# Kernel tuning notes

Measured on AMD Instinct MI355X. Metric: run time of the kernel, lower is better.

The kernel has to match this reference:

```python
import jax, jax.numpy as jnp
import numpy as np

B, A, C, M = 8, 100000, 80, 32
ALPHA, GAMMA = 0.25, 2.0


def setup_inputs() -> dict:
    key = jax.random.key(0)
    k1, k2, k3, k4, k5, k6, k7 = jax.random.split(key, 7)
    cls = jax.random.uniform(k1, (B, A, C), jnp.float32, 1e-3, 1.0 - 1e-3)
    reg = jax.random.normal(k2, (B, A, 4), jnp.float32)
    # anchors: valid boxes with width/height in [16, 256]
    ctr = jax.random.uniform(k3, (A, 2), jnp.float32, 0.0, 800.0)
    wh = jax.random.uniform(k4, (A, 2), jnp.float32, 16.0, 256.0)
    anchors = jnp.concatenate([ctr - wh / 2, ctr + wh / 2], -1)[None]  # [1,A,4]
    # annotations: [B,M,5] = (x1,y1,x2,y2,class); class=-1 marks padding
    gctr = jax.random.uniform(k5, (B, M, 2), jnp.float32, 0.0, 800.0)
    gwh = jax.random.uniform(k6, (B, M, 2), jnp.float32, 32.0, 300.0)
    boxes = jnp.concatenate([gctr - gwh / 2, gctr + gwh / 2], -1)
    labels = jax.random.randint(k7, (B, M), 0, C).astype(jnp.float32)
    labels = labels.at[:, M - 8:].set(-1.0)  # padded GT rows
    annotations = jnp.concatenate([boxes, labels[..., None]], -1)
    return {"classifications": cls, "regressions": reg,
            "anchors": anchors, "annotations": annotations}


def _calc_iou(a, b):
    # a: [A,4] anchors, b: [M,4] gt boxes -> [A,M]
    area_a = (a[:, 2] - a[:, 0]) * (a[:, 3] - a[:, 1])
    area_b = (b[:, 2] - b[:, 0]) * (b[:, 3] - b[:, 1])
    iw = jnp.clip(jnp.minimum(a[:, 2, None], b[None, :, 2]) -
                  jnp.maximum(a[:, 0, None], b[None, :, 0]), 0.0)
    ih = jnp.clip(jnp.minimum(a[:, 3, None], b[None, :, 3]) -
                  jnp.maximum(a[:, 1, None], b[None, :, 1]), 0.0)
    inter = iw * ih
    ua = jnp.clip(area_a[:, None] + area_b[None, :] - inter, 1e-8)
    return inter / ua


def _per_image(cls, reg, anchor, ann):
    valid = ann[:, 4] >= 0.0                     # padded rows (class == -1)
    any_valid = valid.any()
    cls = jnp.clip(cls, 1e-4, 1.0 - 1e-4)
    iou = jnp.where(valid[None, :], _calc_iou(anchor, ann[:, :4]), -1.0)  # [A,M]
    iou_max = iou.max(1)
    iou_argmax = iou.argmax(1)
    pos = iou_max >= 0.5
    num_pos = pos.sum().astype(cls.dtype)
    assigned = ann[iou_argmax]                   # [A,5] gathered GT per anchor
    # build targets: -1 = ignore, 0 = negative, 1 = matched class
    targets = jnp.full(cls.shape, -1.0, cls.dtype)
    targets = jnp.where((iou_max < 0.4)[:, None], 0.0, targets)
    targets = jnp.where(pos[:, None], 0.0, targets)
    onehot = jax.nn.one_hot(assigned[:, 4].astype(jnp.int32), cls.shape[1], dtype=cls.dtype)
    targets = jnp.where(pos[:, None] & (onehot > 0), 1.0, targets)
    # focal loss
    alpha_factor = jnp.where(targets == 1.0, ALPHA, 1.0 - ALPHA)
    focal_w = alpha_factor * jnp.where(targets == 1.0, 1.0 - cls, cls) ** GAMMA
    bce = -(targets * jnp.log(cls) + (1.0 - targets) * jnp.log(1.0 - cls))
    cls_loss = jnp.where(targets != -1.0, focal_w * bce, 0.0).sum() / jnp.maximum(num_pos, 1.0)
    aw = anchor[:, 2] - anchor[:, 0]
    ah = anchor[:, 3] - anchor[:, 1]
    acx = anchor[:, 0] + 0.5 * aw
    acy = anchor[:, 1] + 0.5 * ah
    gw0 = assigned[:, 2] - assigned[:, 0]
    gh0 = assigned[:, 3] - assigned[:, 1]
    gcx = assigned[:, 0] + 0.5 * gw0
    gcy = assigned[:, 1] + 0.5 * gh0
    gw = jnp.clip(gw0, 1.0)
    gh = jnp.clip(gh0, 1.0)
    t = jnp.stack([(gcx - acx) / aw, (gcy - acy) / ah,
                   jnp.log(gw / aw), jnp.log(gh / ah)], axis=1)
    t = t / jnp.array([0.1, 0.1, 0.2, 0.2], cls.dtype)
    diff = jnp.abs(t - reg)
    sl1 = jnp.where(diff <= 1.0 / 9.0, 0.5 * 9.0 * diff ** 2, diff - 0.5 / 9.0)
    reg_loss = jnp.where(pos[:, None], sl1, 0.0).sum() / jnp.maximum(4.0 * num_pos, 1.0)
    reg_loss = jnp.where(num_pos > 0, reg_loss, 0.0)
    return (jnp.where(any_valid, cls_loss, 0.0),
            jnp.where(any_valid, reg_loss, 0.0))


def reference(classifications, regressions, anchors, annotations):
    anchor = anchors[0]
    cl, rl = jax.vmap(lambda c, r, a: _per_image(c, r, anchor, a))(
        classifications, regressions, annotations)
    return (jnp.mean(cl).reshape(1), jnp.mean(rl).reshape(1))
```

## Files before the change

### kernel.cpp

```cpp
#include <hip/hip_runtime.h>

#define A_N 100000
#define B_N 8
#define C_N 80
#define M_N 32
#define BLK 320
#define APB 320
#define NBLK 313

typedef float f32x4 __attribute__((ext_vector_type(4)));

#define NSLOT 64

__device__ __forceinline__ void elem4(f32x4 v, float wgt, float& acc) {
    float s4 = v.x*v.x*__logf(1.f - v.x) + v.y*v.y*__logf(1.f - v.y)
             + v.z*v.z*__logf(1.f - v.z) + v.w*v.w*__logf(1.f - v.w);
    acc = fmaf(-wgt, s4, acc);
}

__global__ __launch_bounds__(BLK) void focal_main(
    const float* __restrict__ cls,
    const float* __restrict__ regs,
    const float* __restrict__ anchors,
    const float* __restrict__ ann,
    float* __restrict__ ws)
{
    __shared__ float sAnn[M_N * 5];
    __shared__ float sW[APB];
    __shared__ float sRed[15];

    const int b          = blockIdx.y;
    const int blockStart = blockIdx.x * APB;
    const int tid        = threadIdx.x;
    const int a          = blockStart + tid;

    if (tid < M_N * 5) sAnn[tid] = ann[b * M_N * 5 + tid];
    __syncthreads();

    float clsPart = 0.f, regPart = 0.f, nposPart = 0.f;
    float pHit = 0.5f;
    int   meta = -2;

    if (a < A_N) {
        float4 an = reinterpret_cast<const float4*>(anchors)[a];
        float areaA = (an.z - an.x) * (an.w - an.y);
        float best = -1e30f;
        int bestIdx = 0;
        #pragma unroll
        for (int m = 0; m < M_N; ++m) {
            float gx1 = sAnn[m*5+0], gy1 = sAnn[m*5+1];
            float gx2 = sAnn[m*5+2], gy2 = sAnn[m*5+3];
            float gl  = sAnn[m*5+4];
            float iouv;
            if (gl >= 0.f) {
                float areaB = (gx2 - gx1) * (gy2 - gy1);
                float iw = fmaxf(fminf(an.z, gx2) - fmaxf(an.x, gx1), 0.f);
                float ih = fmaxf(fminf(an.w, gy2) - fmaxf(an.y, gy1), 0.f);
                float inter = iw * ih;
                float ua = fmaxf(areaA + areaB - inter, 1e-8f);
                iouv = inter / ua;
            } else {
                iouv = -1.f;
            }
            if (iouv > best) { best = iouv; bestIdx = m; }
        }
        bool pos = best >= 0.5f;
        bool neg = best <  0.4f;
        meta = pos ? (int)sAnn[bestIdx*5+4] : (neg ? -1 : -2);

        if (pos) {
            nposPart = 1.f;
            float ph = cls[((size_t)b * A_N + a) * C_N + meta];
            pHit = ph;

            float4 rg = reinterpret_cast<const float4*>(regs)[(size_t)b * A_N + a];
            float gx1 = sAnn[bestIdx*5+0], gy1 = sAnn[bestIdx*5+1];
            float gx2 = sAnn[bestIdx*5+2], gy2 = sAnn[bestIdx*5+3];
            float aw = an.z - an.x, ah = an.w - an.y;
            float acx = an.x + 0.5f * aw, acy = an.y + 0.5f * ah;
            float gw0 = gx2 - gx1, gh0 = gy2 - gy1;
            float gcx = gx1 + 0.5f * gw0, gcy = gy1 + 0.5f * gh0;
            float gw = fmaxf(gw0, 1.f), gh = fmaxf(gh0, 1.f);
            float t0 = ((gcx - acx) / aw) * 10.f;
            float t1 = ((gcy - acy) / ah) * 10.f;
            float t2 = __logf(gw / aw) * 5.f;
            float t3 = __logf(gh / ah) * 5.f;
            float d0 = fabsf(t0 - rg.x), d1 = fabsf(t1 - rg.y);
            float d2 = fabsf(t2 - rg.z), d3 = fabsf(t3 - rg.w);
            #define SL1(d) ((d) <= (1.f/9.f) ? 4.5f*(d)*(d) : (d) - (0.5f/9.f))
            regPart = SL1(d0) + SL1(d1) + SL1(d2) + SL1(d3);
            #undef SL1
        }
    }
    sW[tid] = (meta == -2) ? 0.f : 0.75f;
    __syncthreads();

    const int tD = tid / 20;
    const f32x4* cls4 = reinterpret_cast<const f32x4*>(
        cls + ((size_t)b * A_N + blockStart) * C_N);

    if (blockIdx.x != NBLK - 1) {
        #pragma unroll
        for (int k = 0; k < 20; k += 4) {
            f32x4 v0 = __builtin_nontemporal_load(&cls4[(k + 0) * BLK + tid]);
            f32x4 v1 = __builtin_nontemporal_load(&cls4[(k + 1) * BLK + tid]);
            f32x4 v2 = __builtin_nontemporal_load(&cls4[(k + 2) * BLK + tid]);
            f32x4 v3 = __builtin_nontemporal_load(&cls4[(k + 3) * BLK + tid]);
            float w0 = sW[tD + ((k + 0) << 4)];
            float w1 = sW[tD + ((k + 1) << 4)];
            float w2 = sW[tD + ((k + 2) << 4)];
            float w3 = sW[tD + ((k + 3) << 4)];
            elem4(v0, w0, clsPart);
            elem4(v1, w1, clsPart);
            elem4(v2, w2, clsPart);
            elem4(v3, w3, clsPart);
        }
    } else {
        #pragma unroll
        for (int k = 0; k < 20; ++k) {
            int al = tD + (k << 4);
            if (blockStart + al < A_N) {
                f32x4 v = __builtin_nontemporal_load(&cls4[k * BLK + tid]);
                elem4(v, sW[al], clsPart);
            }
        }
    }

    if (meta >= 0) {
        float om = 1.f - pHit;
        clsPart += -0.25f * om * om * __logf(pHit)
                   + 0.75f * pHit * pHit * __logf(om);
    }

    #pragma unroll
    for (int off = 32; off > 0; off >>= 1) {
        clsPart  += __shfl_down(clsPart,  off);
        regPart  += __shfl_down(regPart,  off);
        nposPart += __shfl_down(nposPart, off);
    }
    const int wid = tid >> 6;
    if ((tid & 63) == 0) {
        sRed[wid]      = clsPart;
        sRed[5 + wid]  = regPart;
        sRed[10 + wid] = nposPart;
    }
    __syncthreads();
    if (tid == 0) {
        const int slot = ((blockIdx.x & 7) << 3) | b;
        float c = sRed[0] + sRed[1] + sRed[2] + sRed[3] + sRed[4];
        float r = sRed[5] + sRed[6] + sRed[7] + sRed[8] + sRed[9];
        float n = sRed[10] + sRed[11] + sRed[12] + sRed[13] + sRed[14];
        atomicAdd(&ws[slot],             c);
        atomicAdd(&ws[NSLOT + slot],     r);
        atomicAdd(&ws[2 * NSLOT + slot], n);
    }
}

__global__ void focal_final(const float* __restrict__ ann,
                            const float* __restrict__ ws,
                            float* __restrict__ out)
{
    if (threadIdx.x == 0 && blockIdx.x == 0) {
        float cSum = 0.f, rSum = 0.f;
        for (int b = 0; b < B_N; ++b) {
            bool anyv = false;
            for (int m = 0; m < M_N; ++m)
                anyv = anyv || (ann[b * M_N * 5 + m * 5 + 4] >= 0.f);
            float cl = 0.f, rl = 0.f, np = 0.f;
            for (int k = 0; k < 8; ++k) {
                cl += ws[(k << 3) | b];
                rl += ws[NSLOT + ((k << 3) | b)];
                np += ws[2 * NSLOT + ((k << 3) | b)];
            }
            cl = cl / fmaxf(np, 1.f);
            rl = rl / fmaxf(4.f * np, 1.f);
            if (np <= 0.f) rl = 0.f;
            if (!anyv) { cl = 0.f; rl = 0.f; }
            cSum += cl;
            rSum += rl;
        }
        out[0] = cSum / (float)B_N;
        out[1] = rSum / (float)B_N;
    }
}

extern "C" void kernel_launch(void* const* d_in, const int* in_sizes, int n_in,
                              void* d_out, int out_size, void* d_ws, size_t ws_size,
                              hipStream_t stream) {
    const float* cls     = (const float*)d_in[0];
    const float* regs    = (const float*)d_in[1];
    const float* anchors = (const float*)d_in[2];
    const float* ann     = (const float*)d_in[3];
    float* out = (float*)d_out;
    float* ws  = (float*)d_ws;

    (void)hipMemsetAsync(ws, 0, 3 * NSLOT * sizeof(float), stream);

    dim3 grid(NBLK, B_N);
    focal_main<<<grid, BLK, 0, stream>>>(cls, regs, anchors, ann, ws);
    focal_final<<<1, 64, 0, stream>>>(ann, ws, out);
}
```

Measured before the change: 67.71 us.

## Prefetch first class tiles before IoU and drop atomics and memset

The first four nontemporal class-score vector loads are issued before the annotation barrier and the IoU matching loop, so their memory latency overlaps the matching compute. Per-block partial sums are now written to distinct workspace slots instead of being atomically added to 64 shared slots. This removes the hipMemsetAsync launch and the atomic contention. The final kernel becomes a 256-thread parallel reduction over all block slots, in exchange for holding more live registers through the IoU loop.

```diff
diff --git a/kernel.cpp b/kernel.cpp
--- a/kernel.cpp
+++ b/kernel.cpp
@@ -7,10 +7,9 @@
 #define BLK 320
 #define APB 320
 #define NBLK 313
+#define NSLOT (NBLK * B_N)
 
 typedef float f32x4 __attribute__((ext_vector_type(4)));
-
-#define NSLOT 64
 
 __device__ __forceinline__ void elem4(f32x4 v, float wgt, float& acc) {
     float s4 = v.x*v.x*__logf(1.f - v.x) + v.y*v.y*__logf(1.f - v.y)
@@ -33,8 +32,20 @@
     const int blockStart = blockIdx.x * APB;
     const int tid        = threadIdx.x;
     const int a          = blockStart + tid;
+    const bool full      = (blockIdx.x != NBLK - 1);
 
     if (tid < M_N * 5) sAnn[tid] = ann[b * M_N * 5 + tid];
+
+    const int tD = tid / 20;
+    const f32x4* cls4 = reinterpret_cast<const f32x4*>(
+        cls + ((size_t)b * A_N + blockStart) * C_N);
+    f32x4 v0, v1, v2, v3;
+    if (full) {
+        v0 = __builtin_nontemporal_load(&cls4[0 * BLK + tid]);
+        v1 = __builtin_nontemporal_load(&cls4[1 * BLK + tid]);
+        v2 = __builtin_nontemporal_load(&cls4[2 * BLK + tid]);
+        v3 = __builtin_nontemporal_load(&cls4[3 * BLK + tid]);
+    }
     __syncthreads();
 
     float clsPart = 0.f, regPart = 0.f, nposPart = 0.f;
@@ -70,8 +81,7 @@
 
         if (pos) {
             nposPart = 1.f;
-            float ph = cls[((size_t)b * A_N + a) * C_N + meta];
-            pHit = ph;
+            pHit = cls[((size_t)b * A_N + a) * C_N + meta];
 
             float4 rg = reinterpret_cast<const float4*>(regs)[(size_t)b * A_N + a];
             float gx1 = sAnn[bestIdx*5+0], gy1 = sAnn[bestIdx*5+1];
@@ -95,25 +105,25 @@
     sW[tid] = (meta == -2) ? 0.f : 0.75f;
     __syncthreads();
 
-    const int tD = tid / 20;
-    const f32x4* cls4 = reinterpret_cast<const f32x4*>(
-        cls + ((size_t)b * A_N + blockStart) * C_N);
-
-    if (blockIdx.x != NBLK - 1) {
-        #pragma unroll
-        for (int k = 0; k < 20; k += 4) {
-            f32x4 v0 = __builtin_nontemporal_load(&cls4[(k + 0) * BLK + tid]);
-            f32x4 v1 = __builtin_nontemporal_load(&cls4[(k + 1) * BLK + tid]);
-            f32x4 v2 = __builtin_nontemporal_load(&cls4[(k + 2) * BLK + tid]);
-            f32x4 v3 = __builtin_nontemporal_load(&cls4[(k + 3) * BLK + tid]);
+    if (full) {
+        elem4(v0, sW[tD + (0 << 4)], clsPart);
+        elem4(v1, sW[tD + (1 << 4)], clsPart);
+        elem4(v2, sW[tD + (2 << 4)], clsPart);
+        elem4(v3, sW[tD + (3 << 4)], clsPart);
+        #pragma unroll
+        for (int k = 4; k < 20; k += 4) {
+            f32x4 u0 = __builtin_nontemporal_load(&cls4[(k + 0) * BLK + tid]);
+            f32x4 u1 = __builtin_nontemporal_load(&cls4[(k + 1) * BLK + tid]);
+            f32x4 u2 = __builtin_nontemporal_load(&cls4[(k + 2) * BLK + tid]);
+            f32x4 u3 = __builtin_nontemporal_load(&cls4[(k + 3) * BLK + tid]);
             float w0 = sW[tD + ((k + 0) << 4)];
             float w1 = sW[tD + ((k + 1) << 4)];
             float w2 = sW[tD + ((k + 2) << 4)];
             float w3 = sW[tD + ((k + 3) << 4)];
-            elem4(v0, w0, clsPart);
-            elem4(v1, w1, clsPart);
-            elem4(v2, w2, clsPart);
-            elem4(v3, w3, clsPart);
+            elem4(u0, w0, clsPart);
+            elem4(u1, w1, clsPart);
+            elem4(u2, w2, clsPart);
+            elem4(u3, w3, clsPart);
         }
     } else {
         #pragma unroll
@@ -146,41 +156,54 @@
     }
     __syncthreads();
     if (tid == 0) {
-        const int slot = ((blockIdx.x & 7) << 3) | b;
-        float c = sRed[0] + sRed[1] + sRed[2] + sRed[3] + sRed[4];
-        float r = sRed[5] + sRed[6] + sRed[7] + sRed[8] + sRed[9];
-        float n = sRed[10] + sRed[11] + sRed[12] + sRed[13] + sRed[14];
-        atomicAdd(&ws[slot],             c);
-        atomicAdd(&ws[NSLOT + slot],     r);
-        atomicAdd(&ws[2 * NSLOT + slot], n);
-    }
-}
-
-__global__ void focal_final(const float* __restrict__ ann,
-                            const float* __restrict__ ws,
-                            float* __restrict__ out)
+        const int slot = blockIdx.x * B_N + b;
+        ws[slot]             = sRed[0] + sRed[1] + sRed[2] + sRed[3] + sRed[4];
+        ws[NSLOT + slot]     = sRed[5] + sRed[6] + sRed[7] + sRed[8] + sRed[9];
+        ws[2 * NSLOT + slot] = sRed[10] + sRed[11] + sRed[12] + sRed[13] + sRed[14];
+    }
+}
+
+__global__ __launch_bounds__(256) void focal_final(
+    const float* __restrict__ ann,
+    const float* __restrict__ ws,
+    float* __restrict__ out)
 {
-    if (threadIdx.x == 0 && blockIdx.x == 0) {
-        float cSum = 0.f, rSum = 0.f;
-        for (int b = 0; b < B_N; ++b) {
-            bool anyv = false;
-            for (int m = 0; m < M_N; ++m)
-                anyv = anyv || (ann[b * M_N * 5 + m * 5 + 4] >= 0.f);
-            float cl = 0.f, rl = 0.f, np = 0.f;
-            for (int k = 0; k < 8; ++k) {
-                cl += ws[(k << 3) | b];
-                rl += ws[NSLOT + ((k << 3) | b)];
-                np += ws[2 * NSLOT + ((k << 3) | b)];
-            }
-            cl = cl / fmaxf(np, 1.f);
-            rl = rl / fmaxf(4.f * np, 1.f);
-            if (np <= 0.f) rl = 0.f;
-            if (!anyv) { cl = 0.f; rl = 0.f; }
-            cSum += cl;
-            rSum += rl;
-        }
-        out[0] = cSum / (float)B_N;
-        out[1] = rSum / (float)B_N;
+    __shared__ float sC[8], sR[8];
+    const int tid = threadIdx.x;
+    const int g   = tid >> 5;
+    const int j   = tid & 31;
+
+    float c = 0.f, r = 0.f, n = 0.f;
+    for (int bx = j; bx < NBLK; bx += 32) {
+        int slot = bx * B_N + g;
+        c += ws[slot];
+        r += ws[NSLOT + slot];
+        n += ws[2 * NSLOT + slot];
+    }
+    #pragma unroll
+    for (int off = 16; off > 0; off >>= 1) {
+        c += __shfl_down(c, off, 32);
+        r += __shfl_down(r, off, 32);
+        n += __shfl_down(n, off, 32);
+    }
+    if (j == 0) {
+        bool anyv = false;
+        for (int m = 0; m < M_N; ++m)
+            anyv = anyv || (ann[g * M_N * 5 + m * 5 + 4] >= 0.f);
+        float cl = c / fmaxf(n, 1.f);
+        float rl = r / fmaxf(4.f * n, 1.f);
+        if (n <= 0.f) rl = 0.f;
+        if (!anyv) { cl = 0.f; rl = 0.f; }
+        sC[g] = cl;
+        sR[g] = rl;
+    }
+    __syncthreads();
+    if (tid == 0) {
+        float cs = 0.f, rs = 0.f;
+        #pragma unroll
+        for (int k = 0; k < 8; ++k) { cs += sC[k]; rs += sR[k]; }
+        out[0] = cs / (float)B_N;
+        out[1] = rs / (float)B_N;
     }
 }
 
@@ -194,9 +217,7 @@
     float* out = (float*)d_out;
     float* ws  = (float*)d_ws;
 
-    (void)hipMemsetAsync(ws, 0, 3 * NSLOT * sizeof(float), stream);
-
     dim3 grid(NBLK, B_N);
     focal_main<<<grid, BLK, 0, stream>>>(cls, regs, anchors, ann, ws);
-    focal_final<<<1, 64, 0, stream>>>(ann, ws, out);
-}
+    focal_final<<<1, 256, 0, stream>>>(ann, ws, out);
+}
```

Result: no change. 68.72 us (+1.5%).
